# Performance work log

Measured on AMD Instinct MI355X. Metric: run time of the kernel, lower is better.

The kernel has to match this reference:

```python
import jax, jax.numpy as jnp
import numpy as np

INPUT_SIZE = 64
HIDDEN = 128
BATCH = 256
SEQ = 2048


def setup_inputs() -> dict:
    key = jax.random.key(0)
    k_x, k_w, k_r = jax.random.split(key, 3)
    x = jax.random.normal(k_x, (BATCH, SEQ, INPUT_SIZE), dtype=jnp.float32)
    # Gate order: i, f, o, z (stacked). W: (4H, I), R: (H, 4H), b: (4H,)
    W = jax.random.normal(k_w, (4 * HIDDEN, INPUT_SIZE), dtype=jnp.float32) * (1.0 / np.sqrt(INPUT_SIZE))
    R = jax.random.normal(k_r, (HIDDEN, 4 * HIDDEN), dtype=jnp.float32) * (1.0 / np.sqrt(HIDDEN))
    b = jnp.zeros((4 * HIDDEN,), dtype=jnp.float32)
    return {"x": x, "W": W, "R": R, "b": b}


def _slstm_scan(x, W, R, b):
    B, S, _ = x.shape
    H = R.shape[0]
    # Precompute input projections for all timesteps: (B, S, 4H)
    pre = jnp.einsum('bsi,gi->bsg', x, W) + b
    pre = jnp.swapaxes(pre, 0, 1)  # (S, B, 4H)

    def step(carry, pre_t):
        h, c, n, m = carry
        gates = pre_t + h @ R  # (B, 4H); note: matmul(h, r), NOT r.T (as in source)
        i_t, f_t, o_t, z_t = jnp.split(gates, 4, axis=-1)
        # log(exp(i_tilda)) == i_tilda; log(sigmoid(f_tilda)) stabilized
        log_f = jax.nn.log_sigmoid(f_t)
        m_new = jnp.maximum(log_f + m, i_t)
        i_p = jnp.exp(i_t - m_new)
        f_p = jnp.exp(log_f + m - m_new)
        c_new = f_p * c + i_p * jnp.tanh(z_t)
        n_new = f_p * n + i_p
        h_new = jax.nn.sigmoid(o_t) * jnp.tanh(c_new / n_new)
        return (h_new, c_new, n_new, m_new), h_new

    z = jnp.zeros((B, H), dtype=x.dtype)
    (_h, _c, _n, _m), hs = jax.lax.scan(step, (z, z, z, z), pre)
    return jnp.swapaxes(hs, 0, 1)  # (B, S, H)


def reference(x, W, R, b):
    return _slstm_scan(x, W, R, b)
```

## Files before the change

### kernel.cpp

```cpp
#include <hip/hip_runtime.h>
#include <hip/hip_fp16.h>

#define BATCH 256
#define SEQ   2048
#define ISZ   64
#define HID   128
#define GATES 512
#define KV    192
#define KT    6

typedef _Float16 f16x8 __attribute__((ext_vector_type(8)));
typedef float    f32x4 __attribute__((ext_vector_type(4)));

__global__ __launch_bounds__(512, 2) void slstm_kernel(
    const float* __restrict__ x, const float* __restrict__ W,
    const float* __restrict__ R, const float* __restrict__ bias,
    float* __restrict__ out)
{
    __shared__ __align__(16) _Float16 vh[2][KV];

    const int t    = threadIdx.x;
    const int lane = t & 63;
    const int w    = t >> 6;
    const int c16  = lane & 15;
    const int g    = lane >> 4;
    const int j    = w * 16 + c16;

    f16x8 bw[4][KT];
#pragma unroll
    for (int q = 0; q < 4; ++q) {
        const int n = q * HID + j;
#pragma unroll
        for (int kt = 0; kt < KT; ++kt) {
            f16x8 v;
#pragma unroll
            for (int e = 0; e < 8; ++e) {
                const int k = kt * 32 + g * 8 + e;
                const float f = (k < ISZ) ? W[n * ISZ + k]
                                          : R[(k - ISZ) * GATES + n];
                v[e] = (_Float16)f;
            }
            bw[q][kt] = v;
        }
    }

    float bb[4];
#pragma unroll
    for (int q = 0; q < 4; ++q) bb[q] = bias[q * HID + j];

    float C_st = 0.f, N_st = 0.f;

    const float* xb   = x   + (size_t)blockIdx.x * SEQ * ISZ;
    float*       outb = out + (size_t)blockIdx.x * SEQ * HID;

    if (t < HID) vh[0][ISZ + t] = (_Float16)0.f;
    float xreg = 0.f;
    if (t < ISZ) {
        vh[0][t] = (_Float16)xb[t];
        xreg = xb[ISZ + t];
    }
    __syncthreads();

    for (int s = 0; s < SEQ; ++s) {
        const _Float16* vcur = vh[s & 1];
        _Float16*       vnxt = vh[(s + 1) & 1];

        const f16x8* va = (const f16x8*)vcur;
        f16x8 af[KT];
#pragma unroll
        for (int kt = 0; kt < KT; ++kt) af[kt] = va[kt * 4 + g];

        f32x4 acc[4] = {{0.f,0.f,0.f,0.f}, {0.f,0.f,0.f,0.f},
                        {0.f,0.f,0.f,0.f}, {0.f,0.f,0.f,0.f}};
#pragma unroll
        for (int kt = 0; kt < KT; ++kt) {
#pragma unroll
            for (int q = 0; q < 4; ++q)
                acc[q] = __builtin_amdgcn_mfma_f32_16x16x32_f16(
                    af[kt], bw[q][kt], acc[q], 0, 0, 0);
        }

        const float gi = acc[0][0] + bb[0];
        const float gf = acc[1][0] + bb[1];
        const float go = acc[2][0] + bb[2];
        const float gz = acc[3][0] + bb[3];

        const float fp = __builtin_amdgcn_rcpf(1.f + __expf(-gf));
        const float ip = __expf(gi);
        const float ez = __expf(2.f * gz);
        const float tz = 1.f - 2.f * __builtin_amdgcn_rcpf(ez + 1.f);
        const float so = __builtin_amdgcn_rcpf(1.f + __expf(-go));

        C_st = fp * C_st + ip * tz;
        N_st = fp * N_st + ip;

        const float ratio = C_st * __builtin_amdgcn_rcpf(N_st);
        const float eh    = __expf(2.f * ratio);
        const float h     = so * (1.f - 2.f * __builtin_amdgcn_rcpf(eh + 1.f));

        if (lane < 16) {
            vnxt[ISZ + j]     = (_Float16)h;
            outb[s * HID + j] = h;
        }
        if (t < ISZ) {
            vnxt[t] = (_Float16)xreg;
            xreg    = (s + 2 < SEQ) ? xb[(s + 2) * ISZ + t] : 0.f;
        }
        __syncthreads();
    }
}

extern "C" void kernel_launch(void* const* d_in, const int* in_sizes, int n_in,
                              void* d_out, int out_size, void* d_ws, size_t ws_size,
                              hipStream_t stream) {
    const float* x = (const float*)d_in[0];
    const float* W = (const float*)d_in[1];
    const float* R = (const float*)d_in[2];
    const float* b = (const float*)d_in[3];
    float* out = (float*)d_out;

    slstm_kernel<<<dim3(BATCH), dim3(512), 0, stream>>>(x, W, R, b, out);
}
```

Baseline: 1.415 ms.

## Process two batch rows per block and fold exp scaling into weights

Each block now runs two independent batch sequences, using 128 blocks instead of 256. Both reuse the same register-resident weight fragments and share one barrier per step, so the two MFMA chains can overlap. Weights and bias are pre-scaled by log2(e) (and 2*log2(e) for the z gate), which lets the activations call exp2 directly without a multiply. The cost is fewer blocks on a GPU with many CUs (256 CUs on MI355X) and more per-thread work each step. The serial per-step latency may still dominate.

```diff
diff --git a/kernel.cpp b/kernel.cpp
--- a/kernel.cpp
+++ b/kernel.cpp
@@ -8,16 +8,24 @@
 #define GATES 512
 #define KV    192
 #define KT    6
+#define NBAT  2
 
 typedef _Float16 f16x8 __attribute__((ext_vector_type(8)));
 typedef float    f32x4 __attribute__((ext_vector_type(4)));
+
+#if __has_builtin(__builtin_amdgcn_exp2f)
+#define EXP2F(v) __builtin_amdgcn_exp2f(v)
+#else
+#define EXP2F(v) exp2f(v)
+#endif
+#define RCPF(v) __builtin_amdgcn_rcpf(v)
 
 __global__ __launch_bounds__(512, 2) void slstm_kernel(
     const float* __restrict__ x, const float* __restrict__ W,
     const float* __restrict__ R, const float* __restrict__ bias,
     float* __restrict__ out)
 {
-    __shared__ __align__(16) _Float16 vh[2][KV];
+    __shared__ __align__(16) _Float16 vh[2][NBAT][KV];
 
     const int t    = threadIdx.x;
     const int lane = t & 63;
@@ -25,6 +33,9 @@
     const int c16  = lane & 15;
     const int g    = lane >> 4;
     const int j    = w * 16 + c16;
+
+    const float L2E = 1.4426950408889634f;
+    const float sc[4] = {L2E, L2E, L2E, 2.0f * L2E};
 
     f16x8 bw[4][KT];
 #pragma unroll
@@ -38,7 +49,7 @@
                 const int k = kt * 32 + g * 8 + e;
                 const float f = (k < ISZ) ? W[n * ISZ + k]
                                           : R[(k - ISZ) * GATES + n];
-                v[e] = (_Float16)f;
+                v[e] = (_Float16)(f * sc[q]);
             }
             bw[q][kt] = v;
         }
@@ -46,65 +57,94 @@
 
     float bb[4];
 #pragma unroll
-    for (int q = 0; q < 4; ++q) bb[q] = bias[q * HID + j];
+    for (int q = 0; q < 4; ++q) bb[q] = bias[q * HID + j] * sc[q];
 
-    float C_st = 0.f, N_st = 0.f;
+    float C0 = 0.f, N0 = 0.f, C1 = 0.f, N1 = 0.f;
 
-    const float* xb   = x   + (size_t)blockIdx.x * SEQ * ISZ;
-    float*       outb = out + (size_t)blockIdx.x * SEQ * HID;
+    const int b0 = 2 * blockIdx.x;
+    const float* xb0 = x + (size_t)b0 * SEQ * ISZ;
+    const float* xb1 = xb0 + (size_t)SEQ * ISZ;
+    float* ob0 = out + (size_t)b0 * SEQ * HID;
+    float* ob1 = ob0 + (size_t)SEQ * HID;
 
-    if (t < HID) vh[0][ISZ + t] = (_Float16)0.f;
+    if (t < NBAT * HID) vh[0][t >> 7][ISZ + (t & 127)] = (_Float16)0.f;
+    const float* myxb = (w == 0) ? xb0 : xb1;
     float xreg = 0.f;
-    if (t < ISZ) {
-        vh[0][t] = (_Float16)xb[t];
-        xreg = xb[ISZ + t];
+    if (w < 2) {
+        vh[0][w][lane] = (_Float16)myxb[lane];
+        xreg = myxb[ISZ + lane];
     }
     __syncthreads();
 
     for (int s = 0; s < SEQ; ++s) {
-        const _Float16* vcur = vh[s & 1];
-        _Float16*       vnxt = vh[(s + 1) & 1];
+        const _Float16* v0 = vh[s & 1][0];
+        const _Float16* v1 = vh[s & 1][1];
+        _Float16* n0p = vh[(s + 1) & 1][0];
+        _Float16* n1p = vh[(s + 1) & 1][1];
 
-        const f16x8* va = (const f16x8*)vcur;
-        f16x8 af[KT];
+        const f16x8* va0 = (const f16x8*)v0;
+        const f16x8* va1 = (const f16x8*)v1;
+        f16x8 af0[KT], af1[KT];
 #pragma unroll
-        for (int kt = 0; kt < KT; ++kt) af[kt] = va[kt * 4 + g];
+        for (int kt = 0; kt < KT; ++kt) {
+            af0[kt] = va0[kt * 4 + g];
+            af1[kt] = va1[kt * 4 + g];
+        }
 
-        f32x4 acc[4] = {{0.f,0.f,0.f,0.f}, {0.f,0.f,0.f,0.f},
-                        {0.f,0.f,0.f,0.f}, {0.f,0.f,0.f,0.f}};
+        f32x4 acc0[4] = {{0.f,0.f,0.f,0.f}, {0.f,0.f,0.f,0.f},
+                         {0.f,0.f,0.f,0.f}, {0.f,0.f,0.f,0.f}};
+        f32x4 acc1[4] = {{0.f,0.f,0.f,0.f}, {0.f,0.f,0.f,0.f},
+                         {0.f,0.f,0.f,0.f}, {0.f,0.f,0.f,0.f}};
 #pragma unroll
         for (int kt = 0; kt < KT; ++kt) {
 #pragma unroll
-            for (int q = 0; q < 4; ++q)
-                acc[q] = __builtin_amdgcn_mfma_f32_16x16x32_f16(
-                    af[kt], bw[q][kt], acc[q], 0, 0, 0);
+            for (int q = 0; q < 4; ++q) {
+                acc0[q] = __builtin_amdgcn_mfma_f32_16x16x32_f16(
+                    af0[kt], bw[q][kt], acc0[q], 0, 0, 0);
+                acc1[q] = __builtin_amdgcn_mfma_f32_16x16x32_f16(
+                    af1[kt], bw[q][kt], acc1[q], 0, 0, 0);
+            }
         }
 
-        const float gi = acc[0][0] + bb[0];
-        const float gf = acc[1][0] + bb[1];
-        const float go = acc[2][0] + bb[2];
-        const float gz = acc[3][0] + bb[3];
+        const float gi0 = acc0[0][0] + bb[0];
+        const float gf0 = acc0[1][0] + bb[1];
+        const float go0 = acc0[2][0] + bb[2];
+        const float gz0 = acc0[3][0] + bb[3];
+        const float fp0 = RCPF(1.f + EXP2F(-gf0));
+        const float ip0 = EXP2F(gi0);
+        const float ez0 = EXP2F(gz0);
+        const float tz0 = 1.f - 2.f * RCPF(ez0 + 1.f);
+        const float so0 = RCPF(1.f + EXP2F(-go0));
+        C0 = fp0 * C0 + ip0 * tz0;
+        N0 = fp0 * N0 + ip0;
+        const float r0 = C0 * RCPF(N0);
+        const float eh0 = EXP2F(2.8853900817779268f * r0);
+        const float h0  = so0 * (1.f - 2.f * RCPF(eh0 + 1.f));
 
-        const float fp = __builtin_amdgcn_rcpf(1.f + __expf(-gf));
-        const float ip = __expf(gi);
-        const float ez = __expf(2.f * gz);
-        const float tz = 1.f - 2.f * __builtin_amdgcn_rcpf(ez + 1.f);
-        const float so = __builtin_amdgcn_rcpf(1.f + __expf(-go));
-
-        C_st = fp * C_st + ip * tz;
-        N_st = fp * N_st + ip;
-
-        const float ratio = C_st * __builtin_amdgcn_rcpf(N_st);
-        const float eh    = __expf(2.f * ratio);
-        const float h     = so * (1.f - 2.f * __builtin_amdgcn_rcpf(eh + 1.f));
+        const float gi1 = acc1[0][0] + bb[0];
+        const float gf1 = acc1[1][0] + bb[1];
+        const float go1 = acc1[2][0] + bb[2];
+        const float gz1 = acc1[3][0] + bb[3];
+        const float fp1 = RCPF(1.f + EXP2F(-gf1));
+        const float ip1 = EXP2F(gi1);
+        const float ez1 = EXP2F(gz1);
+        const float tz1 = 1.f - 2.f * RCPF(ez1 + 1.f);
+        const float so1 = RCPF(1.f + EXP2F(-go1));
+        C1 = fp1 * C1 + ip1 * tz1;
+        N1 = fp1 * N1 + ip1;
+        const float r1 = C1 * RCPF(N1);
+        const float eh1 = EXP2F(2.8853900817779268f * r1);
+        const float h1  = so1 * (1.f - 2.f * RCPF(eh1 + 1.f));
 
         if (lane < 16) {
-            vnxt[ISZ + j]     = (_Float16)h;
-            outb[s * HID + j] = h;
+            n0p[ISZ + j] = (_Float16)h0;
+            n1p[ISZ + j] = (_Float16)h1;
+            ob0[(size_t)s * HID + j] = h0;
+            ob1[(size_t)s * HID + j] = h1;
         }
-        if (t < ISZ) {
-            vnxt[t] = (_Float16)xreg;
-            xreg    = (s + 2 < SEQ) ? xb[(s + 2) * ISZ + t] : 0.f;
+        if (w < 2) {
+            ((w == 0) ? n0p : n1p)[lane] = (_Float16)xreg;
+            xreg = (s + 2 < SEQ) ? myxb[(size_t)(s + 2) * ISZ + lane] : 0.f;
         }
         __syncthreads();
     }
@@ -119,5 +159,5 @@
     const float* b = (const float*)d_in[3];
     float* out = (float*)d_out;
 
-    slstm_kernel<<<dim3(BATCH), dim3(512), 0, stream>>>(x, W, R, b, out);
+    slstm_kernel<<<dim3(BATCH / NBAT), dim3(512), 0, stream>>>(x, W, R, b, out);
 }
```

After: 2.336 ms. +65.1%, slower.
